# Kernel tuning notes

Hardware: AMD Instinct MI355X
Metric: run time of the kernel (lower is better)

Reference implementation:

```python
import math
import jax, jax.numpy as jnp
import numpy as np

H = 1024
N_HALF = 32
DT_MIN, DT_MAX = 0.001, 0.1


def setup_inputs() -> dict:
    key = jax.random.key(0)
    k1, k2 = jax.random.split(key)
    # C ~ complex normal, stored as real view (H, N/2, 2)
    C_param = jax.random.normal(k1, (H, N_HALF, 2), dtype=jnp.float32)
    # log_dt uniform in [log(dt_min), log(dt_max)]
    u = jax.random.uniform(k2, (H,), dtype=jnp.float32)
    log_dt = u * (math.log(DT_MAX) - math.log(DT_MIN)) + math.log(DT_MIN)
    # A real part init: log(0.5); imag part: pi * n, broadcast over h
    log_A_real = jnp.full((H, N_HALF), math.log(0.5), dtype=jnp.float32)
    A_imag = math.pi * jnp.broadcast_to(jnp.arange(N_HALF, dtype=jnp.float32), (H, N_HALF))
    return {
        'C_param': C_param,
        'log_dt': log_dt,
        'log_A_real': log_A_real,
        'A_imag': A_imag,
        'L': 4096,
    }


def reference(C_param, log_dt, log_A_real, A_imag, L):
    dt = jnp.exp(log_dt)                                   # (H,)
    C = C_param[..., 0] + 1j * C_param[..., 1]             # (H, N/2) complex
    A = -jnp.exp(log_A_real) + 1j * A_imag                 # (H, N/2) complex
    dtA = A * dt[:, None]                                  # (H, N/2)
    # Vandermonde: exp(dtA * l) for l = 0..L-1 -> (H, N/2, L)
    K = jnp.exp(dtA[..., None] * jnp.arange(L, dtype=jnp.float32))
    Ceff = C * (jnp.exp(dtA) - 1.0) / A                    # (H, N/2)
    out = 2.0 * jnp.einsum('hn,hnl->hl', Ceff, K).real     # (H, L)
    return out
```

## Files before the change

kernel.cpp:

```cpp
#include <hip/hip_runtime.h>
#include <math.h>


#define H_DIM 1024
#define NHALF 32

template <int CHUNK>
__global__ __launch_bounds__(256) void s4d_kernel(
    const float* __restrict__ C_param,
    const float* __restrict__ log_dt,
    const float* __restrict__ log_A_real,
    const float* __restrict__ A_imag,
    float* __restrict__ out,
    int L)
{
    __shared__ float s_cr[NHALF], s_ci[NHALF];
    __shared__ float s_ar[NHALF], s_ai[NHALF];
    __shared__ float s_sr[NHALF], s_si[NHALF];

    const int h   = blockIdx.x;
    const int tid = threadIdx.x;
    const int stride = 256;

    if (tid < NHALF) {
        const int n = tid;
        const float dt = __expf(log_dt[h]);
        const float Ar = -__expf(log_A_real[h * NHALF + n]);
        const float Ai = A_imag[h * NHALF + n];
        const float ar = Ar * dt;
        const float ai = Ai * dt;
        float es, ec;
        __sincosf(ai, &es, &ec);
        const float em = __expf(ar);
        const float Er = em * ec, Ei = em * es;
        const float nr = Er - 1.0f, ni = Ei;
        const float inv = 1.0f / (Ar * Ar + Ai * Ai);
        const float qr = (nr * Ar + ni * Ai) * inv;
        const float qi = (ni * Ar - nr * Ai) * inv;
        const float Cr = C_param[(h * NHALF + n) * 2 + 0];
        const float Ci = C_param[(h * NHALF + n) * 2 + 1];
        s_cr[n] = Cr * qr - Ci * qi;
        s_ci[n] = Cr * qi + Ci * qr;
        s_ar[n] = ar;
        s_ai[n] = ai;
        float ss, sc;
        __sincosf(ai * (float)stride, &ss, &sc);
        const float sm = __expf(ar * (float)stride);
        s_sr[n] = sm * sc;
        s_si[n] = sm * ss;
    }
    __syncthreads();

    float acc[CHUNK];
#pragma unroll
    for (int k = 0; k < CHUNK; ++k) acc[k] = 0.0f;

    const float t0 = (float)tid;
    for (int n = 0; n < NHALF; ++n) {
        const float cr = s_cr[n], ci = s_ci[n];
        const float ar = s_ar[n], ai = s_ai[n];
        const float sr = s_sr[n], si = s_si[n];
        float zs, zc;
        __sincosf(ai * t0, &zs, &zc);
        const float zm = __expf(ar * t0);
        const float zr = zm * zc, zi = zm * zs;
        float wr = cr * zr - ci * zi;
        float wi = cr * zi + ci * zr;
#pragma unroll
        for (int k = 0; k < CHUNK; ++k) {
            acc[k] += wr;
            const float nwr = fmaf(wr, sr, -wi * si);
            const float nwi = fmaf(wr, si,  wi * sr);
            wr = nwr;
            wi = nwi;
        }
    }

#pragma unroll
    for (int k = 0; k < CHUNK; ++k) {
        out[h * L + tid + k * stride] = 2.0f * acc[k];
    }
}

extern "C" void kernel_launch(void* const* d_in, const int* in_sizes, int n_in,
                              void* d_out, int out_size, void* d_ws, size_t ws_size,
                              hipStream_t stream) {
    const float* C_param    = (const float*)d_in[0];
    const float* log_dt     = (const float*)d_in[1];
    const float* log_A_real = (const float*)d_in[2];
    const float* A_imag     = (const float*)d_in[3];
    float* out = (float*)d_out;

    const int L = out_size / H_DIM;

    s4d_kernel<16><<<dim3(H_DIM), dim3(256), 0, stream>>>(
        C_param, log_dt, log_A_real, A_imag, out, L);
}
```

Before: 85.06 us.

## Split each row across two blocks with dual interleaved recurrences and fast sincos

Each row is now handled by two blocks that each cover half of L. Within a block every thread runs two independent 4-step complex recurrences, one seeded at offset 1024 through a precomputed stride^4 multiplier. This doubles the grid, which helps occupancy, and gives two independent dependency chains for ILP. sincos now uses the native AMDGCN sin/cos after range reduction, and launch bounds request 8 blocks per SM. The launch hardcodes L as a multiple of 2048, so accuracy at large arguments relies on that range reduction.

Result: slower. 89.44 us (+5.1%).

```diff
diff --git a/kernel.cpp b/kernel.cpp
--- a/kernel.cpp
+++ b/kernel.cpp
@@ -5,8 +5,14 @@
 #define H_DIM 1024
 #define NHALF 32
 
-template <int CHUNK>
-__global__ __launch_bounds__(256) void s4d_kernel(
+__device__ __forceinline__ void fast_sincos(float x, float* s, float* c) {
+    float r = x * 0.15915494309189535f;
+    r = r - floorf(r);
+    *s = __builtin_amdgcn_sinf(r);
+    *c = __builtin_amdgcn_cosf(r);
+}
+
+__global__ __launch_bounds__(256, 8) void s4d_kernel(
     const float* __restrict__ C_param,
     const float* __restrict__ log_dt,
     const float* __restrict__ log_A_real,
@@ -17,10 +23,11 @@
     __shared__ float s_cr[NHALF], s_ci[NHALF];
     __shared__ float s_ar[NHALF], s_ai[NHALF];
     __shared__ float s_sr[NHALF], s_si[NHALF];
+    __shared__ float s_gr[NHALF], s_gi[NHALF];
 
-    const int h   = blockIdx.x;
-    const int tid = threadIdx.x;
-    const int stride = 256;
+    const int h    = blockIdx.x >> 1;
+    const int half = blockIdx.x & 1;
+    const int tid  = threadIdx.x;
 
     if (tid < NHALF) {
         const int n = tid;
@@ -30,7 +37,7 @@
         const float ar = Ar * dt;
         const float ai = Ai * dt;
         float es, ec;
-        __sincosf(ai, &es, &ec);
+        fast_sincos(ai, &es, &ec);
         const float em = __expf(ar);
         const float Er = em * ec, Ei = em * es;
         const float nr = Er - 1.0f, ni = Ei;
@@ -44,41 +51,57 @@
         s_ar[n] = ar;
         s_ai[n] = ai;
         float ss, sc;
-        __sincosf(ai * (float)stride, &ss, &sc);
-        const float sm = __expf(ar * (float)stride);
-        s_sr[n] = sm * sc;
-        s_si[n] = sm * ss;
+        fast_sincos(ai * 256.0f, &ss, &sc);
+        const float sm = __expf(ar * 256.0f);
+        const float sr = sm * sc, si = sm * ss;
+        s_sr[n] = sr;
+        s_si[n] = si;
+        const float s512r = sr * sr - si * si;
+        const float s512i = 2.0f * sr * si;
+        s_gr[n] = s512r * s512r - s512i * s512i;
+        s_gi[n] = 2.0f * s512r * s512i;
     }
     __syncthreads();
 
-    float acc[CHUNK];
-#pragma unroll
-    for (int k = 0; k < CHUNK; ++k) acc[k] = 0.0f;
+    float accA[4] = {0.0f, 0.0f, 0.0f, 0.0f};
+    float accB[4] = {0.0f, 0.0f, 0.0f, 0.0f};
 
-    const float t0 = (float)tid;
+    const float t0 = (float)(half * 2048 + tid);
+
     for (int n = 0; n < NHALF; ++n) {
+        const float sr = s_sr[n], si = s_si[n];
+        const float gr = s_gr[n], gi = s_gi[n];
         const float cr = s_cr[n], ci = s_ci[n];
         const float ar = s_ar[n], ai = s_ai[n];
-        const float sr = s_sr[n], si = s_si[n];
+
         float zs, zc;
-        __sincosf(ai * t0, &zs, &zc);
+        fast_sincos(ai * t0, &zs, &zc);
         const float zm = __expf(ar * t0);
         const float zr = zm * zc, zi = zm * zs;
-        float wr = cr * zr - ci * zi;
-        float wi = cr * zi + ci * zr;
+
+        float aWr = cr * zr - ci * zi;
+        float aWi = cr * zi + ci * zr;
+        float bWr = aWr * gr - aWi * gi;
+        float bWi = aWr * gi + aWi * gr;
+
 #pragma unroll
-        for (int k = 0; k < CHUNK; ++k) {
-            acc[k] += wr;
-            const float nwr = fmaf(wr, sr, -wi * si);
-            const float nwi = fmaf(wr, si,  wi * sr);
-            wr = nwr;
-            wi = nwi;
+        for (int k = 0; k < 4; ++k) {
+            accA[k] += aWr;
+            accB[k] += bWr;
+            const float nAr = fmaf(aWr, sr, -(aWi * si));
+            const float nAi = fmaf(aWr, si,  (aWi * sr));
+            const float nBr = fmaf(bWr, sr, -(bWi * si));
+            const float nBi = fmaf(bWr, si,  (bWi * sr));
+            aWr = nAr; aWi = nAi;
+            bWr = nBr; bWi = nBi;
         }
     }
 
+    float* o = out + h * L + half * 2048 + tid;
 #pragma unroll
-    for (int k = 0; k < CHUNK; ++k) {
-        out[h * L + tid + k * stride] = 2.0f * acc[k];
+    for (int k = 0; k < 4; ++k) {
+        o[k * 256]        = 2.0f * accA[k];
+        o[k * 256 + 1024] = 2.0f * accB[k];
     }
 }
 
@@ -92,7 +115,8 @@
     float* out = (float*)d_out;
 
     const int L = out_size / H_DIM;
+    const int halves = L / 2048;
 
-    s4d_kernel<16><<<dim3(H_DIM), dim3(256), 0, stream>>>(
+    s4d_kernel<<<dim3(H_DIM * halves), dim3(256), 0, stream>>>(
         C_param, log_dt, log_A_real, A_imag, out, L);
 }
```
